# Performance work log

Measured on AMD Instinct MI355X. Metric: run time of the kernel, lower is better.

## Reference

```python
import jax, jax.numpy as jnp
import numpy as np

B, T1, S, M = 64, 129, 128, 32   # batch, time-major dim, seq_len, num_series
U = 256                           # SkipGRUUnits
SKIP = 4                          # skip
HW = 128                          # highway window (== S by shape constraints)


def _skip_lstm(x_seq, kernel, rkernel, kernel2, bias, bias2, s0, units, skip):
    """Run the bespoke skip-LSTM cell over time. x_seq: (B, T, D) -> (B, T, U)."""
    Bx = x_seq.shape[0]
    # precompute input projections for all timesteps: (B, T, 4U)
    xW = jnp.einsum('btd,du->btu', x_seq, kernel) + bias
    # recurrent kernel viewed per-gate: Rk[:, g, :] == rkernel[:, g*U:(g+1)*U]
    Rk = rkernel.reshape(units, 4, units)

    def step(carry, x_t):
        h_tm1, c_tm1, prev_h = carry            # (B,4U), (B,U), (B,U*skip)
        x_i, x_f, x_c, x_o = jnp.split(x_t, 4, axis=1)
        hg = h_tm1.reshape(Bx, 4, units)        # gate-specific previous state
        r = jnp.einsum('bgu,ugv->bgv', hg, Rk)  # (B,4,U)
        i = jax.nn.sigmoid(x_i + r[:, 0])
        f = jax.nn.sigmoid(x_f + r[:, 1])
        c = f * c_tm1 + i * jnp.tanh(x_c + r[:, 2])
        o = jax.nn.sigmoid(x_o + r[:, 3])
        h = o * jnp.tanh(c)
        h_skip = jax.nn.sigmoid(prev_h[:, :units] @ kernel2 + bias2)
        h = s0 * h + (1.0 - s0) * h_skip
        new_h_tm1 = jnp.concatenate([i, f, c, o], axis=1)
        new_prev = jnp.concatenate([prev_h[:, units:], h], axis=1)
        return (new_h_tm1, c, new_prev), h

    init = (jnp.zeros((Bx, 4 * units), x_seq.dtype),
            jnp.zeros((Bx, units), x_seq.dtype),
            jnp.zeros((Bx, units * skip), x_seq.dtype))
    _, hs = jax.lax.scan(step, init, jnp.swapaxes(xW, 0, 1))  # (T,B,U)
    return jnp.swapaxes(hs, 0, 1)


def setup_inputs() -> dict:
    key = jax.random.key(0)
    ks = jax.random.split(key, 10)
    g = lambda k, shape, s=0.05: (jax.random.normal(k, shape, jnp.float32) * s)
    return {
        'X': jax.random.normal(ks[0], (B, T1, S, M), jnp.float32),
        'enc_kernel': g(ks[1], (M, 4 * U)),
        'enc_rkernel': g(ks[2], (U, 4 * U)),
        'enc_kernel2': g(ks[3], (U, U)),
        'enc_bias': jnp.zeros((4 * U,), jnp.float32),
        'enc_bias2': jnp.zeros((U,), jnp.float32),
        'enc_s0': jnp.float32(0.5),
        'dec_kernel': g(ks[4], (U, 4 * U)),
        'dec_rkernel': g(ks[5], (U, 4 * U)),
        'dec_kernel2': g(ks[6], (U, U)),
        'dec_bias': jnp.zeros((4 * U,), jnp.float32),
        'dec_bias2': jnp.zeros((U,), jnp.float32),
        'dec_s0': jnp.float32(0.5),
        'dense_w': g(ks[7], (S * U, S * M), 0.01),
        'dense_b': jnp.zeros((S * M,), jnp.float32),
        'final_w': g(ks[8], (HW,), 0.05),
        'final_b': jnp.zeros((), jnp.float32),
    }


def reference(X, enc_kernel, enc_rkernel, enc_kernel2, enc_bias, enc_bias2, enc_s0,
              dec_kernel, dec_rkernel, dec_kernel2, dec_bias, dec_bias2, dec_s0,
              dense_w, dense_b, final_w, final_b):
    X1 = X[:, 0]        # (B, S, M) encoder input
    X2 = X[:, 1:]       # (B, T1-1, S, M) highway inputs
    SE = _skip_lstm(X1, enc_kernel, enc_rkernel, enc_kernel2, enc_bias, enc_bias2, enc_s0, U, SKIP)
    SD = _skip_lstm(SE, dec_kernel, dec_rkernel, dec_kernel2, dec_bias, dec_bias2, dec_s0, U, SKIP)
    RD = SD.reshape(X.shape[0], S * U)
    Y = (RD @ dense_w + dense_b).reshape(-1, S, M)  # (B, S, M)
    # highway: PreARTrans takes last HW steps, shared final Linear(S->1) over time axis
    Z2 = jnp.einsum('bism,s->bim', X2[:, :, -HW:, :], final_w) + final_b  # (B, T1-1, M)
    return Y + Z2
```

## Files before the change

### kernel.cpp

```cpp
#include <hip/hip_runtime.h>
#include <hip/hip_fp16.h>


__device__ __forceinline__ float sigmoidf_(float x) {
    return 1.0f / (1.0f + __expf(-x));
}
__device__ __forceinline__ float tanhf_(float x) {
    float xc = fminf(fmaxf(x, -15.f), 15.f);
    float e = __expf(2.f * xc);
    return (e - 1.f) / (e + 1.f);
}
__device__ __forceinline__ unsigned pkh(float lo, float hi) {
    __half2 h = __halves2half2(__float2half(lo), __float2half(hi));
    return *reinterpret_cast<unsigned*>(&h);
}
__device__ __forceinline__ float2 uph(unsigned u) {
    __half2 h = *reinterpret_cast<__half2*>(&u);
    return __half22float2(h);
}

__global__ __launch_bounds__(256) void packall(
    const float* __restrict__ e_rk, const float* __restrict__ d_rk,
    const float* __restrict__ d_k,  const float* __restrict__ e_k,
    const float* __restrict__ e_k2, const float* __restrict__ d_k2,
    float4* __restrict__ rk4e, float4* __restrict__ rk4d,
    float4* __restrict__ dk4,  float4* __restrict__ ek4,
    unsigned* __restrict__ kh2e, unsigned* __restrict__ kh2d,
    unsigned* __restrict__ flags)
{
    const int bx = blockIdx.x, v = threadIdx.x;
    if (bx < 800) {
        const float* src; float4* dst; int row;
        if (bx < 256)      { src = e_rk; dst = rk4e; row = bx; }
        else if (bx < 512) { src = d_rk; dst = rk4d; row = bx - 256; }
        else if (bx < 768) { src = d_k;  dst = dk4;  row = bx - 512; }
        else               { src = e_k;  dst = ek4;  row = bx - 768; }
        const float* s = src + (size_t)row * 1024;
        dst[row * 256 + v] = make_float4(s[v], s[256 + v], s[512 + v], s[768 + v]);
    } else if (bx < 928) {
        const int u2 = bx - 800;
        kh2e[u2 * 256 + v] = pkh(e_k2[(2 * u2) * 256 + v], e_k2[(2 * u2 + 1) * 256 + v]);
        kh2d[u2 * 256 + v] = pkh(d_k2[(2 * u2) * 256 + v], d_k2[(2 * u2 + 1) * 256 + v]);
    } else {
        flags[v] = 0u;
    }
}

__global__ __launch_bounds__(256) void xw_gemm_enc(
    const float*  __restrict__ X,
    const float4* __restrict__ ek4,
    const float*  __restrict__ bias,
    float4* __restrict__ xWp)
{
    const int v = threadIdx.x;
    const int r0 = blockIdx.x * 16;
    __shared__ float se[16][32];

    #pragma unroll
    for (int p = 0; p < 2; ++p) {
        int idx = p * 256 + v;
        int rr = idx >> 5, d = idx & 31;
        int R = r0 + rr, b = R >> 7, t = R & 127;
        se[rr][d] = X[((size_t)b * 129 * 128 + t) * 32 + d];
    }
    __syncthreads();

    float4 bv = make_float4(bias[v], bias[256 + v], bias[512 + v], bias[768 + v]);
    float4 acc[16];
    #pragma unroll
    for (int rr = 0; rr < 16; ++rr) acc[rr] = bv;

    #pragma unroll
    for (int u = 0; u < 32; ++u) {
        float4 w = ek4[u * 256 + v];
        #pragma unroll
        for (int rr = 0; rr < 16; ++rr) {
            float s = se[rr][u];
            acc[rr].x += s * w.x; acc[rr].y += s * w.y;
            acc[rr].z += s * w.z; acc[rr].w += s * w.w;
        }
    }
    #pragma unroll
    for (int rr = 0; rr < 16; ++rr)
        xWp[(size_t)(r0 + rr) * 256 + v] = acc[rr];
}

__global__ __launch_bounds__(512) void xw_gemm_dec(
    const float*  __restrict__ SE,
    const float4* __restrict__ dk4,
    const float*  __restrict__ bias,
    float4* __restrict__ xWp)
{
    const int tid = threadIdx.x;
    const int v = tid & 255;
    const int hh = tid >> 8;
    const int rbase = blockIdx.x * 32;
    __shared__ float se[32][256];

    for (int i = tid; i < 8192; i += 512) {
        int rr = i >> 8, c = i & 255;
        se[rr][c] = SE[(size_t)(rbase + rr) * 256 + c];
    }
    __syncthreads();

    float4 bv = make_float4(bias[v], bias[256 + v], bias[512 + v], bias[768 + v]);
    float4 acc[16];
    #pragma unroll
    for (int rr = 0; rr < 16; ++rr) acc[rr] = bv;

    #pragma unroll 8
    for (int u = 0; u < 256; ++u) {
        float4 w = dk4[u * 256 + v];
        #pragma unroll
        for (int rr = 0; rr < 16; ++rr) {
            float s = se[hh * 16 + rr][u];
            acc[rr].x += s * w.x; acc[rr].y += s * w.y;
            acc[rr].z += s * w.z; acc[rr].w += s * w.w;
        }
    }
    #pragma unroll
    for (int rr = 0; rr < 16; ++rr)
        xWp[(size_t)(rbase + hh * 16 + rr) * 256 + v] = acc[rr];
}

__global__ __launch_bounds__(1024, 4) void rec9(
    const float4*   __restrict__ xW,
    const float4*   __restrict__ rk4,
    const unsigned* __restrict__ kh2,
    const float*    __restrict__ bias2,
    const float*    __restrict__ s0p,
    float* __restrict__ out,
    float* __restrict__ EX,
    unsigned* __restrict__ flags,
    unsigned fbase)
{
    const int b     = blockIdx.x & 63;
    const int slice = blockIdx.x >> 6;
    const int voff  = slice * 64;
    const int tid   = threadIdx.x;
    const int us    = tid >> 6;
    const int vl    = tid & 63;
    const int v     = voff + vl;

    __shared__ float4 wres[128][64];
    __shared__ float4 pA[16][64];
    __shared__ float  pS[16][64];
    __shared__ float4 h4[256];
    __shared__ float  pq[4][256];

    for (int i = tid; i < 8192; i += 1024) {
        int r = i >> 6, vv = i & 63;
        int cc = r >> 3, j = r & 7;
        wres[r][vv] = rk4[(cc * 16 + j) * 256 + voff + vv];
    }
    float4 wreg[8];
    unsigned kreg[8];
    {
        const float4*   wp = rk4 + (us * 16 + 8) * 256 + v;
        const unsigned* kp = kh2 + (us * 8) * 256 + v;
        #pragma unroll
        for (int j = 0; j < 8; ++j) wreg[j] = wp[j * 256];
        #pragma unroll
        for (int j = 0; j < 8; ++j) kreg[j] = kp[j * 256];
    }
    if (tid < 256) {
        h4[tid] = make_float4(0.f, 0.f, 0.f, 0.f);
        pq[0][tid] = 0.f; pq[1][tid] = 0.f; pq[2][tid] = 0.f; pq[3][tid] = 0.f;
    }
    float cst = 0.f;
    const float s0 = s0p[0];
    const float b2 = bias2[voff + vl];
    unsigned* mflag = flags + b * 4 + slice;
    __syncthreads();

    for (int t = 0; t < 128; ++t) {
        float4 xa = make_float4(0.f, 0.f, 0.f, 0.f);
        if (tid < 64) xa = xW[((size_t)b * 128 + t) * 256 + voff + tid];
        if (t > 0 && tid < 3) {
            int ps = tid + (tid >= slice ? 1 : 0);
            const unsigned* pf = flags + b * 4 + ps;
            while (__hip_atomic_load(pf, __ATOMIC_RELAXED, __HIP_MEMORY_SCOPE_AGENT) < fbase + (unsigned)t)
                __builtin_amdgcn_s_sleep(2);
        }
        __syncthreads();
        if (t > 0) {
            const int sp = (t + 1) & 1;
            if (tid < 480) {
                int pi = tid / 160;
                int j  = tid - pi * 160;
                int ps = pi + (pi >= slice ? 1 : 0);
                const unsigned long long* src = (const unsigned long long*)
                    (EX + (((size_t)sp * 64 + b) * 4 + ps) * 320);
                unsigned long long d = __hip_atomic_load(src + j, __ATOMIC_RELAXED, __HIP_MEMORY_SCOPE_AGENT);
                if (j < 128) {
                    reinterpret_cast<unsigned long long*>(&h4[ps * 64])[j] = d;
                } else {
                    int k = j - 128;
                    union { unsigned long long u; float f[2]; } cv; cv.u = d;
                    pq[(t + 3) & 3][ps * 64 + 2 * k]     = cv.f[0];
                    pq[(t + 3) & 3][ps * 64 + 2 * k + 1] = cv.f[1];
                }
            }
        }
        __syncthreads();

        float ai = 0.f, af = 0.f, acg = 0.f, ao = 0.f, as = 0.f;
        const int slot = t & 3;
        #pragma unroll
        for (int j = 0; j < 8; ++j) {
            float4 w = wres[us * 8 + j][vl];
            float4 g = h4[us * 16 + j];
            ai += g.x * w.x; af += g.y * w.y; acg += g.z * w.z; ao += g.w * w.w;
        }
        #pragma unroll
        for (int j = 0; j < 8; ++j) {
            float4 w = wreg[j];
            float4 g = h4[us * 16 + 8 + j];
            ai += g.x * w.x; af += g.y * w.y; acg += g.z * w.z; ao += g.w * w.w;
        }
        #pragma unroll
        for (int j = 0; j < 8; ++j) {
            float2 kk = uph(kreg[j]);
            as += pq[slot][us * 16 + 2 * j] * kk.x + pq[slot][us * 16 + 2 * j + 1] * kk.y;
        }
        pA[us][vl] = make_float4(ai, af, acg, ao);
        pS[us][vl] = as;
        __syncthreads();

        if (tid < 64) {
            float4 A = pA[0][vl];
            float  S = pS[0][vl];
            #pragma unroll
            for (int cc = 1; cc < 16; ++cc) {
                float4 q = pA[cc][vl];
                A.x += q.x; A.y += q.y; A.z += q.z; A.w += q.w;
                S += pS[cc][vl];
            }
            float gi = sigmoidf_(xa.x + A.x);
            float gf = sigmoidf_(xa.y + A.y);
            float cb = tanhf_(xa.z + A.z);
            cst = gf * cst + gi * cb;
            float go = sigmoidf_(xa.w + A.w);
            float hh = go * tanhf_(cst);
            float hs = sigmoidf_(S + b2);
            float hf = s0 * hh + (1.f - s0) * hs;
            h4[voff + vl] = make_float4(gi, gf, cst, go);
            pq[slot][voff + vl] = hf;
            out[((size_t)b * 128 + t) * 256 + voff + vl] = hf;
            float* dst = EX + (((size_t)(t & 1) * 64 + b) * 4 + slice) * 320;
            union { float4 f4; unsigned long long u[2]; } gv;
            gv.f4 = make_float4(gi, gf, cst, go);
            __hip_atomic_store((unsigned long long*)dst + 2 * vl,     gv.u[0], __ATOMIC_RELAXED, __HIP_MEMORY_SCOPE_AGENT);
            __hip_atomic_store((unsigned long long*)dst + 2 * vl + 1, gv.u[1], __ATOMIC_RELAXED, __HIP_MEMORY_SCOPE_AGENT);
            __hip_atomic_store(dst + 256 + vl, hf, __ATOMIC_RELAXED, __HIP_MEMORY_SCOPE_AGENT);
        }
        __syncthreads();
        if (tid == 0)
            __hip_atomic_store(mflag, fbase + (unsigned)(t + 1), __ATOMIC_RELAXED, __HIP_MEMORY_SCOPE_AGENT);
    }
}

__global__ __launch_bounds__(512, 4) void dense3(
    const float* __restrict__ SD,
    const float* __restrict__ dw,
    float* __restrict__ P)
{
    const int bid = blockIdx.x;
    const int kc = bid >> 5;
    const int bb = (bid >> 3) & 3;
    const int ct = bid & 7;
    const int tid = threadIdx.x;
    const int wv  = tid >> 6;
    const int wvj = wv & 1;
    const int wv2 = wv >> 1;
    const int lane = tid & 63;
    const int j0 = ct * 512 + wvj * 256 + lane * 4;
    const int kbase = kc * 2048;

    __shared__ float sst[16][68];
    __shared__ float red[4][4][520];

    float4 acc[16];
    #pragma unroll
    for (int b = 0; b < 16; ++b) acc[b] = make_float4(0.f, 0.f, 0.f, 0.f);

    for (int k0 = 0; k0 < 2048; k0 += 64) {
        if (tid < 256) {
            int r = tid >> 4, c4 = (tid & 15) * 4;
            float4 s4 = *reinterpret_cast<const float4*>(
                SD + (size_t)(bb * 16 + r) * 32768 + kbase + k0 + c4);
            sst[r][c4] = s4.x; sst[r][c4 + 1] = s4.y; sst[r][c4 + 2] = s4.z; sst[r][c4 + 3] = s4.w;
        }
        __syncthreads();
        #pragma unroll 2
        for (int kk = 0; kk < 16; ++kk) {
            const int krel = kk * 4 + wv2;
            float4 w4 = *reinterpret_cast<const float4*>(
                dw + (size_t)(kbase + k0 + krel) * 4096 + j0);
            #pragma unroll
            for (int b = 0; b < 16; ++b) {
                float s = sst[b][krel];
                acc[b].x += s * w4.x; acc[b].y += s * w4.y;
                acc[b].z += s * w4.z; acc[b].w += s * w4.w;
            }
        }
        __syncthreads();
    }

    for (int bg = 0; bg < 4; ++bg) {
        __syncthreads();
        #pragma unroll
        for (int i = 0; i < 4; ++i) {
            float4 a = acc[bg * 4 + i];
            float* d = &red[wv2][i][wvj * 256 + lane * 4];
            d[0] = a.x; d[1] = a.y; d[2] = a.z; d[3] = a.w;
        }
        __syncthreads();
        {
            int bi = tid >> 7;
            int jj = (tid & 127) * 4;
            float4 s;
            s.x = red[0][bi][jj]     + red[1][bi][jj]     + red[2][bi][jj]     + red[3][bi][jj];
            s.y = red[0][bi][jj + 1] + red[1][bi][jj + 1] + red[2][bi][jj + 1] + red[3][bi][jj + 1];
            s.z = red[0][bi][jj + 2] + red[1][bi][jj + 2] + red[2][bi][jj + 2] + red[3][bi][jj + 2];
            s.w = red[0][bi][jj + 3] + red[1][bi][jj + 3] + red[2][bi][jj + 3] + red[3][bi][jj + 3];
            *reinterpret_cast<float4*>(
                P + ((size_t)(kc * 64 + bb * 16 + bg * 4 + bi) * 4096) + ct * 512 + jj) = s;
        }
    }
}

__global__ __launch_bounds__(256) void reduce_z2(
    const float* __restrict__ P,
    const float* __restrict__ db,
    const float* __restrict__ X,
    const float* __restrict__ fw,
    const float* __restrict__ fbp,
    float* __restrict__ out)
{
    const int o4 = blockIdx.x * 256 + threadIdx.x;
    const int b  = o4 >> 10;
    const int j4 = o4 & 1023;
    const int j0 = j4 * 4;
    const int i  = j0 >> 5;
    const int m  = j0 & 31;

    float4 acc = *reinterpret_cast<const float4*>(db + j0);
    #pragma unroll
    for (int kc = 0; kc < 16; ++kc) {
        float4 p = *reinterpret_cast<const float4*>(P + (size_t)(kc * 64 + b) * 4096 + j0);
        acc.x += p.x; acc.y += p.y; acc.z += p.z; acc.w += p.w;
    }

    const float* xp = X + ((size_t)(b * 129 + 1 + i) * 128) * 32 + m;
    #pragma unroll 8
    for (int s = 0; s < 128; ++s) {
        float4 xv = *reinterpret_cast<const float4*>(xp + (size_t)s * 32);
        float w = fw[s];
        acc.x += w * xv.x; acc.y += w * xv.y; acc.z += w * xv.z; acc.w += w * xv.w;
    }
    const float fb = fbp[0];
    acc.x += fb; acc.y += fb; acc.z += fb; acc.w += fb;
    *reinterpret_cast<float4*>(out + (size_t)o4 * 4) = acc;
}

extern "C" void kernel_launch(void* const* d_in, const int* in_sizes, int n_in,
                              void* d_out, int out_size, void* d_ws, size_t ws_size,
                              hipStream_t stream) {
    const float* X    = (const float*)d_in[0];
    const float* e_k  = (const float*)d_in[1];
    const float* e_rk = (const float*)d_in[2];
    const float* e_k2 = (const float*)d_in[3];
    const float* e_b  = (const float*)d_in[4];
    const float* e_b2 = (const float*)d_in[5];
    const float* e_s0 = (const float*)d_in[6];
    const float* d_k  = (const float*)d_in[7];
    const float* d_rk = (const float*)d_in[8];
    const float* d_k2 = (const float*)d_in[9];
    const float* d_b  = (const float*)d_in[10];
    const float* d_b2 = (const float*)d_in[11];
    const float* d_s0 = (const float*)d_in[12];
    const float* dw   = (const float*)d_in[13];
    const float* db   = (const float*)d_in[14];
    const float* fw   = (const float*)d_in[15];
    const float* fb   = (const float*)d_in[16];

    float* ws = (float*)d_ws;
    float4*   rk4e  = (float4*)(ws);
    float4*   rk4d  = (float4*)(ws + 262144);
    float4*   dk4   = (float4*)(ws + 524288);
    float4*   ek4   = (float4*)(ws + 786432);
    unsigned* kh2e  = (unsigned*)(ws + 819200);
    unsigned* kh2d  = (unsigned*)(ws + 851968);
    float*    EX    = ws + 884736;
    unsigned* flags = (unsigned*)(ws + 1212416);
    float*    xW    = ws + 1310720;
    float*    SE    = ws + 9699328;
    float*    SD    = ws + 11796480;

    float* P = xW;

    hipLaunchKernelGGL(packall, dim3(929), dim3(256), 0, stream,
                       e_rk, d_rk, d_k, e_k, e_k2, d_k2,
                       rk4e, rk4d, dk4, ek4, kh2e, kh2d, flags);
    hipLaunchKernelGGL(xw_gemm_enc, dim3(512), dim3(256), 0, stream,
                       X, ek4, e_b, (float4*)xW);
    hipLaunchKernelGGL(rec9, dim3(256), dim3(1024), 0, stream,
                       (const float4*)xW, rk4e, kh2e, e_b2, e_s0, SE, EX, flags, 0u);
    hipLaunchKernelGGL(xw_gemm_dec, dim3(256), dim3(512), 0, stream,
                       SE, dk4, d_b, (float4*)xW);
    hipLaunchKernelGGL(rec9, dim3(256), dim3(1024), 0, stream,
                       (const float4*)xW, rk4d, kh2d, d_b2, d_s0, SD, EX, flags, 128u);
    hipLaunchKernelGGL(dense3, dim3(512), dim3(512), 0, stream, SD, dw, P);
    hipLaunchKernelGGL(reduce_z2, dim3(256), dim3(256), 0, stream,
                       P, db, X, fw, fb, (float*)d_out);
}
```

Before: 1.191 ms.

## Split recurrence across 8 blocks per batch pair and interleave two batches

The recurrent kernel now gives each block two batch elements and a 32-column slice, so each batch is spread over 8 blocks instead of 4. Work for the two batches is software-pipelined: while one batch's gate update and state exchange are in flight, the other batch's matvec runs. The aim is to hide cross-block flag waits and global exchange latency behind compute. It also moves most recurrent weights and the packed skip kernel into shared memory and replaces the block-wide wait with per-producer readiness flags in shared memory. The cost is more producers per batch to synchronise with and more complex spin-wait logic.

```diff
diff --git a/kernel.cpp b/kernel.cpp
--- a/kernel.cpp
+++ b/kernel.cpp
@@ -42,7 +42,7 @@
         kh2e[u2 * 256 + v] = pkh(e_k2[(2 * u2) * 256 + v], e_k2[(2 * u2 + 1) * 256 + v]);
         kh2d[u2 * 256 + v] = pkh(d_k2[(2 * u2) * 256 + v], d_k2[(2 * u2 + 1) * 256 + v]);
     } else {
-        flags[v] = 0u;
+        flags[(bx - 928) * 256 + v] = 0u;
     }
 }
 
@@ -123,7 +123,7 @@
         xWp[(size_t)(rbase + hh * 16 + rr) * 256 + v] = acc[rr];
 }
 
-__global__ __launch_bounds__(1024, 4) void rec9(
+__global__ __launch_bounds__(1024, 4) void rec10(
     const float4*   __restrict__ xW,
     const float4*   __restrict__ rk4,
     const unsigned* __restrict__ kh2,
@@ -134,129 +134,167 @@
     unsigned* __restrict__ flags,
     unsigned fbase)
 {
-    const int b     = blockIdx.x & 63;
-    const int slice = blockIdx.x >> 6;
-    const int voff  = slice * 64;
+    const int p     = blockIdx.x & 31;
+    const int slice = blockIdx.x >> 5;
+    const int voff  = slice * 32;
     const int tid   = threadIdx.x;
-    const int us    = tid >> 6;
-    const int vl    = tid & 63;
+    const int uc    = tid >> 5;
+    const int vl    = tid & 31;
     const int v     = voff + vl;
-
-    __shared__ float4 wres[128][64];
-    __shared__ float4 pA[16][64];
-    __shared__ float  pS[16][64];
-    __shared__ float4 h4[256];
-    __shared__ float  pq[4][256];
-
-    for (int i = tid; i < 8192; i += 1024) {
-        int r = i >> 6, vv = i & 63;
-        int cc = r >> 3, j = r & 7;
-        wres[r][vv] = rk4[(cc * 16 + j) * 256 + voff + vv];
-    }
+    const int b0    = 2 * p, b1 = 2 * p + 1;
+
+    __shared__ float4   wres[192][32];
+    __shared__ unsigned kh2l[128][32];
+    __shared__ float4   h4[2][256];
+    __shared__ float    pq[2][4][256];
+    __shared__ float4   pA[32][33];
+    __shared__ float    pS[32][33];
+    __shared__ unsigned sready[2][8];
+
+    for (int i = tid; i < 6144; i += 1024) {
+        int r = i >> 5, vv = i & 31;
+        wres[r][vv] = rk4[r * 256 + voff + vv];
+    }
+    for (int i = tid; i < 4096; i += 1024) {
+        int r = i >> 5, vv = i & 31;
+        kh2l[r][vv] = kh2[r * 256 + voff + vv];
+    }
+    if (tid < 512) {
+        int c = tid >> 8, u = tid & 255;
+        h4[c][u] = make_float4(0.f, 0.f, 0.f, 0.f);
+        pq[c][0][u] = 0.f; pq[c][1][u] = 0.f; pq[c][2][u] = 0.f; pq[c][3][u] = 0.f;
+    }
+    if (tid < 16) sready[tid >> 3][tid & 7] = 0u;
+
     float4 wreg[8];
-    unsigned kreg[8];
-    {
-        const float4*   wp = rk4 + (us * 16 + 8) * 256 + v;
-        const unsigned* kp = kh2 + (us * 8) * 256 + v;
-        #pragma unroll
-        for (int j = 0; j < 8; ++j) wreg[j] = wp[j * 256];
-        #pragma unroll
-        for (int j = 0; j < 8; ++j) kreg[j] = kp[j * 256];
-    }
-    if (tid < 256) {
-        h4[tid] = make_float4(0.f, 0.f, 0.f, 0.f);
-        pq[0][tid] = 0.f; pq[1][tid] = 0.f; pq[2][tid] = 0.f; pq[3][tid] = 0.f;
-    }
-    float cst = 0.f;
+    if (uc >= 24) {
+        #pragma unroll
+        for (int j = 0; j < 8; ++j)
+            wreg[j] = rk4[(uc * 8 + j) * 256 + v];
+    }
+    float cst0 = 0.f, cst1 = 0.f;
+    float4 xa0 = make_float4(0.f,0.f,0.f,0.f), xa1 = xa0;
     const float s0 = s0p[0];
-    const float b2 = bias2[voff + vl];
-    unsigned* mflag = flags + b * 4 + slice;
+    const float b2 = bias2[v];
     __syncthreads();
 
     for (int t = 0; t < 128; ++t) {
-        float4 xa = make_float4(0.f, 0.f, 0.f, 0.f);
-        if (tid < 64) xa = xW[((size_t)b * 128 + t) * 256 + voff + tid];
-        if (t > 0 && tid < 3) {
-            int ps = tid + (tid >= slice ? 1 : 0);
-            const unsigned* pf = flags + b * 4 + ps;
-            while (__hip_atomic_load(pf, __ATOMIC_RELAXED, __HIP_MEMORY_SCOPE_AGENT) < fbase + (unsigned)t)
-                __builtin_amdgcn_s_sleep(2);
-        }
-        __syncthreads();
-        if (t > 0) {
-            const int sp = (t + 1) & 1;
-            if (tid < 480) {
-                int pi = tid / 160;
-                int j  = tid - pi * 160;
-                int ps = pi + (pi >= slice ? 1 : 0);
-                const unsigned long long* src = (const unsigned long long*)
-                    (EX + (((size_t)sp * 64 + b) * 4 + ps) * 320);
-                unsigned long long d = __hip_atomic_load(src + j, __ATOMIC_RELAXED, __HIP_MEMORY_SCOPE_AGENT);
-                if (j < 128) {
-                    reinterpret_cast<unsigned long long*>(&h4[ps * 64])[j] = d;
-                } else {
-                    int k = j - 128;
-                    union { unsigned long long u; float f[2]; } cv; cv.u = d;
-                    pq[(t + 3) & 3][ps * 64 + 2 * k]     = cv.f[0];
-                    pq[(t + 3) & 3][ps * 64 + 2 * k + 1] = cv.f[1];
+        #pragma unroll
+        for (int c = 0; c < 2; ++c) {
+            const int bc = 2 * p + c;
+            const int bo = 2 * p + (c ^ 1);
+            if (tid < 32) {
+                const int tf = t - (c == 0 ? 1 : 0);
+                if (tf >= 0) {
+                    float4 A = pA[0][tid]; float S = pS[0][tid];
+                    #pragma unroll
+                    for (int cc = 1; cc < 32; ++cc) {
+                        float4 q = pA[cc][tid];
+                        A.x += q.x; A.y += q.y; A.z += q.z; A.w += q.w;
+                        S += pS[cc][tid];
+                    }
+                    float4 xa = (c == 0) ? xa1 : xa0;
+                    float gi = sigmoidf_(xa.x + A.x);
+                    float gf = sigmoidf_(xa.y + A.y);
+                    float cb = tanhf_(xa.z + A.z);
+                    float cstn = gf * ((c == 0) ? cst1 : cst0) + gi * cb;
+                    if (c == 0) cst1 = cstn; else cst0 = cstn;
+                    float go = sigmoidf_(xa.w + A.w);
+                    float hh = go * tanhf_(cstn);
+                    float hs = sigmoidf_(S + b2);
+                    float hf = s0 * hh + (1.f - s0) * hs;
+                    h4[c ^ 1][voff + tid] = make_float4(gi, gf, cstn, go);
+                    pq[c ^ 1][tf & 3][voff + tid] = hf;
+                    out[((size_t)bo * 128 + tf) * 256 + voff + tid] = hf;
+                    float* dst = EX + (((size_t)(tf & 1) * 64 + bo) * 8 + slice) * 160;
+                    union { float4 f4; unsigned long long u[2]; } gv;
+                    gv.f4 = make_float4(gi, gf, cstn, go);
+                    __hip_atomic_store((unsigned long long*)dst + 2 * tid,     gv.u[0], __ATOMIC_RELAXED, __HIP_MEMORY_SCOPE_AGENT);
+                    __hip_atomic_store((unsigned long long*)dst + 2 * tid + 1, gv.u[1], __ATOMIC_RELAXED, __HIP_MEMORY_SCOPE_AGENT);
+                    __hip_atomic_store((unsigned*)(dst + 128) + tid, __float_as_uint(hf), __ATOMIC_RELAXED, __HIP_MEMORY_SCOPE_AGENT);
+                    asm volatile("s_waitcnt vmcnt(0)" ::: "memory");
+                    if (tid == 0)
+                        __hip_atomic_store(flags + bo * 8 + slice, fbase + (unsigned)(tf + 1),
+                                           __ATOMIC_RELAXED, __HIP_MEMORY_SCOPE_AGENT);
+                }
+                float4 x = xW[((size_t)bc * 128 + t) * 256 + voff + tid];
+                if (c == 0) xa0 = x; else xa1 = x;
+            } else if (t > 0) {
+                const int st = tid - 64;
+                const unsigned T = fbase + (unsigned)t;
+                if (tid >= 64 && st < 7) {
+                    int ps = st + (st >= slice ? 1 : 0);
+                    const unsigned* pf = flags + bc * 8 + ps;
+                    while (__hip_atomic_load(pf, __ATOMIC_RELAXED, __HIP_MEMORY_SCOPE_AGENT) < T)
+                        __builtin_amdgcn_s_sleep(1);
+                    __hip_atomic_store(&sready[c][ps], T, __ATOMIC_RELAXED, __HIP_MEMORY_SCOPE_WORKGROUP);
+                }
+                if (tid >= 64 && st < 560) {
+                    int pi = st / 80, j = st - pi * 80;
+                    int ps = pi + (pi >= slice ? 1 : 0);
+                    while (__hip_atomic_load(&sready[c][ps], __ATOMIC_RELAXED, __HIP_MEMORY_SCOPE_WORKGROUP) < T)
+                        __builtin_amdgcn_s_sleep(1);
+                    const unsigned long long* src = (const unsigned long long*)
+                        (EX + (((size_t)((t + 1) & 1) * 64 + bc) * 8 + ps) * 160);
+                    unsigned long long d = __hip_atomic_load(src + j, __ATOMIC_RELAXED, __HIP_MEMORY_SCOPE_AGENT);
+                    if (j < 64) {
+                        ((unsigned long long*)&h4[c][0])[ps * 64 + j] = d;
+                    } else {
+                        int k = j - 64;
+                        union { unsigned long long u; float f[2]; } cv; cv.u = d;
+                        pq[c][(t + 3) & 3][ps * 32 + 2 * k]     = cv.f[0];
+                        pq[c][(t + 3) & 3][ps * 32 + 2 * k + 1] = cv.f[1];
+                    }
                 }
             }
-        }
-        __syncthreads();
-
-        float ai = 0.f, af = 0.f, acg = 0.f, ao = 0.f, as = 0.f;
-        const int slot = t & 3;
-        #pragma unroll
-        for (int j = 0; j < 8; ++j) {
-            float4 w = wres[us * 8 + j][vl];
-            float4 g = h4[us * 16 + j];
-            ai += g.x * w.x; af += g.y * w.y; acg += g.z * w.z; ao += g.w * w.w;
-        }
-        #pragma unroll
-        for (int j = 0; j < 8; ++j) {
-            float4 w = wreg[j];
-            float4 g = h4[us * 16 + 8 + j];
-            ai += g.x * w.x; af += g.y * w.y; acg += g.z * w.z; ao += g.w * w.w;
-        }
-        #pragma unroll
-        for (int j = 0; j < 8; ++j) {
-            float2 kk = uph(kreg[j]);
-            as += pq[slot][us * 16 + 2 * j] * kk.x + pq[slot][us * 16 + 2 * j + 1] * kk.y;
-        }
-        pA[us][vl] = make_float4(ai, af, acg, ao);
-        pS[us][vl] = as;
-        __syncthreads();
-
-        if (tid < 64) {
-            float4 A = pA[0][vl];
-            float  S = pS[0][vl];
-            #pragma unroll
-            for (int cc = 1; cc < 16; ++cc) {
-                float4 q = pA[cc][vl];
-                A.x += q.x; A.y += q.y; A.z += q.z; A.w += q.w;
-                S += pS[cc][vl];
+            __syncthreads();
+            {
+                const int slot = t & 3;
+                const int u0 = uc * 8;
+                float ai = 0.f, af = 0.f, ac = 0.f, ao = 0.f, as = 0.f;
+                if (uc < 24) {
+                    #pragma unroll
+                    for (int j = 0; j < 8; ++j) {
+                        float4 w = wres[u0 + j][vl];
+                        float4 g = h4[c][u0 + j];
+                        ai += g.x * w.x; af += g.y * w.y; ac += g.z * w.z; ao += g.w * w.w;
+                    }
+                } else {
+                    #pragma unroll
+                    for (int j = 0; j < 8; ++j) {
+                        float4 w = wreg[j];
+                        float4 g = h4[c][u0 + j];
+                        ai += g.x * w.x; af += g.y * w.y; ac += g.z * w.z; ao += g.w * w.w;
+                    }
+                }
+                #pragma unroll
+                for (int jp = 0; jp < 4; ++jp) {
+                    float2 kk = uph(kh2l[uc * 4 + jp][vl]);
+                    as += pq[c][slot][u0 + 2 * jp] * kk.x + pq[c][slot][u0 + 2 * jp + 1] * kk.y;
+                }
+                pA[uc][vl] = make_float4(ai, af, ac, ao);
+                pS[uc][vl] = as;
             }
-            float gi = sigmoidf_(xa.x + A.x);
-            float gf = sigmoidf_(xa.y + A.y);
-            float cb = tanhf_(xa.z + A.z);
-            cst = gf * cst + gi * cb;
-            float go = sigmoidf_(xa.w + A.w);
-            float hh = go * tanhf_(cst);
-            float hs = sigmoidf_(S + b2);
-            float hf = s0 * hh + (1.f - s0) * hs;
-            h4[voff + vl] = make_float4(gi, gf, cst, go);
-            pq[slot][voff + vl] = hf;
-            out[((size_t)b * 128 + t) * 256 + voff + vl] = hf;
-            float* dst = EX + (((size_t)(t & 1) * 64 + b) * 4 + slice) * 320;
-            union { float4 f4; unsigned long long u[2]; } gv;
-            gv.f4 = make_float4(gi, gf, cst, go);
-            __hip_atomic_store((unsigned long long*)dst + 2 * vl,     gv.u[0], __ATOMIC_RELAXED, __HIP_MEMORY_SCOPE_AGENT);
-            __hip_atomic_store((unsigned long long*)dst + 2 * vl + 1, gv.u[1], __ATOMIC_RELAXED, __HIP_MEMORY_SCOPE_AGENT);
-            __hip_atomic_store(dst + 256 + vl, hf, __ATOMIC_RELAXED, __HIP_MEMORY_SCOPE_AGENT);
-        }
-        __syncthreads();
-        if (tid == 0)
-            __hip_atomic_store(mflag, fbase + (unsigned)(t + 1), __ATOMIC_RELAXED, __HIP_MEMORY_SCOPE_AGENT);
+            __syncthreads();
+        }
+    }
+    if (tid < 32) {
+        float4 A = pA[0][tid]; float S = pS[0][tid];
+        #pragma unroll
+        for (int cc = 1; cc < 32; ++cc) {
+            float4 q = pA[cc][tid];
+            A.x += q.x; A.y += q.y; A.z += q.z; A.w += q.w;
+            S += pS[cc][tid];
+        }
+        float gi = sigmoidf_(xa1.x + A.x);
+        float gf = sigmoidf_(xa1.y + A.y);
+        float cb = tanhf_(xa1.z + A.z);
+        cst1 = gf * cst1 + gi * cb;
+        float go = sigmoidf_(xa1.w + A.w);
+        float hh = go * tanhf_(cst1);
+        float hs = sigmoidf_(S + b2);
+        float hf = s0 * hh + (1.f - s0) * hs;
+        out[((size_t)b1 * 128 + 127) * 256 + voff + tid] = hf;
     }
 }
 
@@ -393,24 +431,24 @@
     unsigned* kh2e  = (unsigned*)(ws + 819200);
     unsigned* kh2d  = (unsigned*)(ws + 851968);
     float*    EX    = ws + 884736;
-    unsigned* flags = (unsigned*)(ws + 1212416);
+    unsigned* flags = (unsigned*)(ws + 1048576);
     float*    xW    = ws + 1310720;
     float*    SE    = ws + 9699328;
     float*    SD    = ws + 11796480;
 
     float* P = xW;
 
-    hipLaunchKernelGGL(packall, dim3(929), dim3(256), 0, stream,
+    hipLaunchKernelGGL(packall, dim3(930), dim3(256), 0, stream,
                        e_rk, d_rk, d_k, e_k, e_k2, d_k2,
                        rk4e, rk4d, dk4, ek4, kh2e, kh2d, flags);
     hipLaunchKernelGGL(xw_gemm_enc, dim3(512), dim3(256), 0, stream,
                        X, ek4, e_b, (float4*)xW);
-    hipLaunchKernelGGL(rec9, dim3(256), dim3(1024), 0, stream,
+    hipLaunchKernelGGL(rec10, dim3(256), dim3(1024), 0, stream,
                        (const float4*)xW, rk4e, kh2e, e_b2, e_s0, SE, EX, flags, 0u);
     hipLaunchKernelGGL(xw_gemm_dec, dim3(256), dim3(512), 0, stream,
                        SE, dk4, d_b, (float4*)xW);
-    hipLaunchKernelGGL(rec9, dim3(256), dim3(1024), 0, stream,
-                       (const float4*)xW, rk4d, kh2d, d_b2, d_s0, SD, EX, flags, 128u);
+    hipLaunchKernelGGL(rec10, dim3(256), dim3(1024), 0, stream,
+                       (const float4*)xW, rk4d, kh2d, d_b2, d_s0, SD, EX, flags, 1000u);
     hipLaunchKernelGGL(dense3, dim3(512), dim3(512), 0, stream, SD, dw, P);
     hipLaunchKernelGGL(reduce_z2, dim3(256), dim3(256), 0, stream,
                        P, db, X, fw, fb, (float*)d_out);
```

New measurement: 1.605 ms. 1.35x slower.

## Double-buffer SD tile and prefetch dense weights in registers

Applied to the files above, without the earlier changes.

The dense GEMM kernel now double-buffers the SD activation tile in shared memory, so the next chunk loads while the current one is computed, removing one barrier per iteration. It also keeps 8 float4 weight rows in flight in registers and issues each load ahead of the FMAs that consume it, to hide global memory latency on the large weight stream. The cost is more shared memory and higher register pressure under launch_bounds(512,4), which could cause spills or lower occupancy.

```diff
diff --git a/kernel.cpp b/kernel.cpp
--- a/kernel.cpp
+++ b/kernel.cpp
@@ -260,7 +260,7 @@
     }
 }
 
-__global__ __launch_bounds__(512, 4) void dense3(
+__global__ __launch_bounds__(512, 4) void dense4(
     const float* __restrict__ SD,
     const float* __restrict__ dw,
     float* __restrict__ P)
@@ -277,31 +277,56 @@
     const int j0 = ct * 512 + wvj * 256 + lane * 4;
     const int kbase = kc * 2048;
 
-    __shared__ float sst[16][68];
+    __shared__ float sst[2][16][68];
     __shared__ float red[4][4][520];
 
     float4 acc[16];
     #pragma unroll
     for (int b = 0; b < 16; ++b) acc[b] = make_float4(0.f, 0.f, 0.f, 0.f);
 
-    for (int k0 = 0; k0 < 2048; k0 += 64) {
-        if (tid < 256) {
-            int r = tid >> 4, c4 = (tid & 15) * 4;
+    const int sr = tid >> 4, sc4 = (tid & 15) * 4;
+    if (tid < 256) {
+        float4 s4 = *reinterpret_cast<const float4*>(
+            SD + (size_t)(bb * 16 + sr) * 32768 + kbase + sc4);
+        float* d = &sst[0][sr][0];
+        d[sc4] = s4.x; d[sc4 + 1] = s4.y; d[sc4 + 2] = s4.z; d[sc4 + 3] = s4.w;
+    }
+    __syncthreads();
+
+    for (int it = 0; it < 32; ++it) {
+        const int buf = it & 1;
+        const int k0 = it * 64;
+        if (it < 31 && tid < 256) {
             float4 s4 = *reinterpret_cast<const float4*>(
-                SD + (size_t)(bb * 16 + r) * 32768 + kbase + k0 + c4);
-            sst[r][c4] = s4.x; sst[r][c4 + 1] = s4.y; sst[r][c4 + 2] = s4.z; sst[r][c4 + 3] = s4.w;
-        }
-        __syncthreads();
-        #pragma unroll 2
-        for (int kk = 0; kk < 16; ++kk) {
-            const int krel = kk * 4 + wv2;
-            float4 w4 = *reinterpret_cast<const float4*>(
-                dw + (size_t)(kbase + k0 + krel) * 4096 + j0);
+                SD + (size_t)(bb * 16 + sr) * 32768 + kbase + k0 + 64 + sc4);
+            float* d = &sst[buf ^ 1][sr][0];
+            d[sc4] = s4.x; d[sc4 + 1] = s4.y; d[sc4 + 2] = s4.z; d[sc4 + 3] = s4.w;
+        }
+        const float* wrow = dw + (size_t)(kbase + k0 + wv2) * 4096 + j0;
+        float4 wa[4], wb[4];
+        #pragma unroll
+        for (int q = 0; q < 4; ++q)
+            wa[q] = *reinterpret_cast<const float4*>(wrow + (size_t)(q * 4) * 4096);
+        #pragma unroll
+        for (int q = 0; q < 4; ++q)
+            wb[q] = *reinterpret_cast<const float4*>(wrow + (size_t)(16 + q * 4) * 4096);
+        #pragma unroll
+        for (int g = 0; g < 4; ++g) {
             #pragma unroll
-            for (int b = 0; b < 16; ++b) {
-                float s = sst[b][krel];
-                acc[b].x += s * w4.x; acc[b].y += s * w4.y;
-                acc[b].z += s * w4.z; acc[b].w += s * w4.w;
+            for (int q = 0; q < 4; ++q) {
+                const int krel = (g * 4 + q) * 4 + wv2;
+                float4 w4 = (g & 1) ? wb[q] : wa[q];
+                #pragma unroll
+                for (int b = 0; b < 16; ++b) {
+                    float s = sst[buf][b][krel];
+                    acc[b].x += s * w4.x; acc[b].y += s * w4.y;
+                    acc[b].z += s * w4.z; acc[b].w += s * w4.w;
+                }
+                if (g < 2) {
+                    float4 nw = *reinterpret_cast<const float4*>(
+                        wrow + (size_t)((g + 2) * 16 + q * 4) * 4096);
+                    if (g & 1) wb[q] = nw; else wa[q] = nw;
+                }
             }
         }
         __syncthreads();
@@ -411,7 +436,7 @@
                        SE, dk4, d_b, (float4*)xW);
     hipLaunchKernelGGL(rec9, dim3(256), dim3(1024), 0, stream,
                        (const float4*)xW, rk4d, kh2d, d_b2, d_s0, SD, EX, flags, 128u);
-    hipLaunchKernelGGL(dense3, dim3(512), dim3(512), 0, stream, SD, dw, P);
+    hipLaunchKernelGGL(dense4, dim3(512), dim3(512), 0, stream, SD, dw, P);
     hipLaunchKernelGGL(reduce_z2, dim3(256), dim3(256), 0, stream,
                        P, db, X, fw, fb, (float*)d_out);
 }
```

Result: no change. 1.207 ms (+1.3%).

## Replace block-wide barriers with per-slice LDS ready flags in recurrent kernel

Applied to the files above, without the earlier changes.

The recurrent kernel stops using two __syncthreads per step around the cross-block exchange. One polling wave spins on the peer flags and publishes a per-peer ready value in shared memory. Each group of four waves that consumes a given peer's slice waits only on that peer's flag, loads the data, and then starts its partial dot products. The producer wave now publishes its own flag right after a vmcnt wait, which drops one more barrier. The aim is to cut per-step barrier latency on this serial 128-step chain, at the cost of busy-wait spinning and reliance on LDS memory-ordering subtleties.

```diff
diff --git a/kernel.cpp b/kernel.cpp
--- a/kernel.cpp
+++ b/kernel.cpp
@@ -123,7 +123,7 @@
         xWp[(size_t)(rbase + hh * 16 + rr) * 256 + v] = acc[rr];
 }
 
-__global__ __launch_bounds__(1024, 4) void rec9(
+__global__ __launch_bounds__(1024, 4) void rec11(
     const float4*   __restrict__ xW,
     const float4*   __restrict__ rk4,
     const unsigned* __restrict__ kh2,
@@ -141,12 +141,16 @@
     const int us    = tid >> 6;
     const int vl    = tid & 63;
     const int v     = voff + vl;
+    const int reg   = us >> 2;
+    const bool own  = (reg == slice);
+    const int lane  = vl;
 
     __shared__ float4 wres[128][64];
     __shared__ float4 pA[16][64];
     __shared__ float  pS[16][64];
     __shared__ float4 h4[256];
     __shared__ float  pq[4][256];
+    __shared__ unsigned sready[4];
 
     for (int i = tid; i < 8192; i += 1024) {
         int r = i >> 6, vv = i & 63;
@@ -167,64 +171,70 @@
         h4[tid] = make_float4(0.f, 0.f, 0.f, 0.f);
         pq[0][tid] = 0.f; pq[1][tid] = 0.f; pq[2][tid] = 0.f; pq[3][tid] = 0.f;
     }
+    if (tid < 4) sready[tid] = fbase;
     float cst = 0.f;
     const float s0 = s0p[0];
     const float b2 = bias2[voff + vl];
     unsigned* mflag = flags + b * 4 + slice;
+    const bool pollwave = (us == slice * 4 + 1);
     __syncthreads();
 
     for (int t = 0; t < 128; ++t) {
+        const unsigned T = fbase + (unsigned)t;
         float4 xa = make_float4(0.f, 0.f, 0.f, 0.f);
         if (tid < 64) xa = xW[((size_t)b * 128 + t) * 256 + voff + tid];
-        if (t > 0 && tid < 3) {
-            int ps = tid + (tid >= slice ? 1 : 0);
-            const unsigned* pf = flags + b * 4 + ps;
-            while (__hip_atomic_load(pf, __ATOMIC_RELAXED, __HIP_MEMORY_SCOPE_AGENT) < fbase + (unsigned)t)
-                __builtin_amdgcn_s_sleep(2);
-        }
-        __syncthreads();
+
         if (t > 0) {
-            const int sp = (t + 1) & 1;
-            if (tid < 480) {
-                int pi = tid / 160;
-                int j  = tid - pi * 160;
-                int ps = pi + (pi >= slice ? 1 : 0);
-                const unsigned long long* src = (const unsigned long long*)
-                    (EX + (((size_t)sp * 64 + b) * 4 + ps) * 320);
-                unsigned long long d = __hip_atomic_load(src + j, __ATOMIC_RELAXED, __HIP_MEMORY_SCOPE_AGENT);
-                if (j < 128) {
-                    reinterpret_cast<unsigned long long*>(&h4[ps * 64])[j] = d;
-                } else {
-                    int k = j - 128;
-                    union { unsigned long long u; float f[2]; } cv; cv.u = d;
-                    pq[(t + 3) & 3][ps * 64 + 2 * k]     = cv.f[0];
-                    pq[(t + 3) & 3][ps * 64 + 2 * k + 1] = cv.f[1];
+            if (pollwave && lane < 3) {
+                int ps = lane + (lane >= slice ? 1 : 0);
+                const unsigned* pf = flags + b * 4 + ps;
+                while (__hip_atomic_load(pf, __ATOMIC_RELAXED, __HIP_MEMORY_SCOPE_AGENT) < T) { }
+                __hip_atomic_store(&sready[ps], T, __ATOMIC_RELAXED, __HIP_MEMORY_SCOPE_WORKGROUP);
+            }
+            if (!own) {
+                while (__hip_atomic_load(&sready[reg], __ATOMIC_RELAXED, __HIP_MEMORY_SCOPE_WORKGROUP) < T)
+                    __builtin_amdgcn_s_sleep(1);
+                const int sp = (t + 1) & 1;
+                const float* srcf = EX + (((size_t)sp * 64 + b) * 4 + reg) * 320;
+                if (lane < 32) {
+                    const unsigned long long* src = (const unsigned long long*)srcf;
+                    int jj = (us & 3) * 32 + lane;
+                    unsigned long long d = __hip_atomic_load(src + jj, __ATOMIC_RELAXED, __HIP_MEMORY_SCOPE_AGENT);
+                    reinterpret_cast<unsigned long long*>(&h4[reg * 64])[(us & 3) * 32 + lane] = d;
+                } else if (lane < 48) {
+                    int k = lane - 32;
+                    int uu = (us & 3) * 16 + k;
+                    unsigned hv = __hip_atomic_load((const unsigned*)(srcf + 256) + uu,
+                                                    __ATOMIC_RELAXED, __HIP_MEMORY_SCOPE_AGENT);
+                    pq[(t + 3) & 3][reg * 64 + uu] = __uint_as_float(hv);
                 }
-            }
-        }
-        __syncthreads();
-
-        float ai = 0.f, af = 0.f, acg = 0.f, ao = 0.f, as = 0.f;
-        const int slot = t & 3;
-        #pragma unroll
-        for (int j = 0; j < 8; ++j) {
-            float4 w = wres[us * 8 + j][vl];
-            float4 g = h4[us * 16 + j];
-            ai += g.x * w.x; af += g.y * w.y; acg += g.z * w.z; ao += g.w * w.w;
-        }
-        #pragma unroll
-        for (int j = 0; j < 8; ++j) {
-            float4 w = wreg[j];
-            float4 g = h4[us * 16 + 8 + j];
-            ai += g.x * w.x; af += g.y * w.y; acg += g.z * w.z; ao += g.w * w.w;
-        }
-        #pragma unroll
-        for (int j = 0; j < 8; ++j) {
-            float2 kk = uph(kreg[j]);
-            as += pq[slot][us * 16 + 2 * j] * kk.x + pq[slot][us * 16 + 2 * j + 1] * kk.y;
-        }
-        pA[us][vl] = make_float4(ai, af, acg, ao);
-        pS[us][vl] = as;
+                asm volatile("s_waitcnt vmcnt(0) lgkmcnt(0)" ::: "memory");
+            }
+        }
+
+        {
+            float ai = 0.f, af = 0.f, acg = 0.f, ao = 0.f, as = 0.f;
+            const int slot = t & 3;
+            #pragma unroll
+            for (int j = 0; j < 8; ++j) {
+                float4 w = wres[us * 8 + j][vl];
+                float4 g = h4[us * 16 + j];
+                ai += g.x * w.x; af += g.y * w.y; acg += g.z * w.z; ao += g.w * w.w;
+            }
+            #pragma unroll
+            for (int j = 0; j < 8; ++j) {
+                float4 w = wreg[j];
+                float4 g = h4[us * 16 + 8 + j];
+                ai += g.x * w.x; af += g.y * w.y; acg += g.z * w.z; ao += g.w * w.w;
+            }
+            #pragma unroll
+            for (int j = 0; j < 8; ++j) {
+                float2 kk = uph(kreg[j]);
+                as += pq[slot][us * 16 + 2 * j] * kk.x + pq[slot][us * 16 + 2 * j + 1] * kk.y;
+            }
+            pA[us][vl] = make_float4(ai, af, acg, ao);
+            pS[us][vl] = as;
+        }
         __syncthreads();
 
         if (tid < 64) {
@@ -245,18 +255,19 @@
             float hs = sigmoidf_(S + b2);
             float hf = s0 * hh + (1.f - s0) * hs;
             h4[voff + vl] = make_float4(gi, gf, cst, go);
-            pq[slot][voff + vl] = hf;
+            pq[t & 3][voff + vl] = hf;
             out[((size_t)b * 128 + t) * 256 + voff + vl] = hf;
             float* dst = EX + (((size_t)(t & 1) * 64 + b) * 4 + slice) * 320;
             union { float4 f4; unsigned long long u[2]; } gv;
             gv.f4 = make_float4(gi, gf, cst, go);
             __hip_atomic_store((unsigned long long*)dst + 2 * vl,     gv.u[0], __ATOMIC_RELAXED, __HIP_MEMORY_SCOPE_AGENT);
             __hip_atomic_store((unsigned long long*)dst + 2 * vl + 1, gv.u[1], __ATOMIC_RELAXED, __HIP_MEMORY_SCOPE_AGENT);
-            __hip_atomic_store(dst + 256 + vl, hf, __ATOMIC_RELAXED, __HIP_MEMORY_SCOPE_AGENT);
-        }
-        __syncthreads();
-        if (tid == 0)
-            __hip_atomic_store(mflag, fbase + (unsigned)(t + 1), __ATOMIC_RELAXED, __HIP_MEMORY_SCOPE_AGENT);
+            __hip_atomic_store((unsigned*)(dst + 256) + vl, __float_as_uint(hf), __ATOMIC_RELAXED, __HIP_MEMORY_SCOPE_AGENT);
+            asm volatile("s_waitcnt vmcnt(0)" ::: "memory");
+            if (tid == 0)
+                __hip_atomic_store(mflag, T + 1u, __ATOMIC_RELAXED, __HIP_MEMORY_SCOPE_AGENT);
+        }
+        __syncthreads();
     }
 }
 
@@ -405,11 +416,11 @@
                        rk4e, rk4d, dk4, ek4, kh2e, kh2d, flags);
     hipLaunchKernelGGL(xw_gemm_enc, dim3(512), dim3(256), 0, stream,
                        X, ek4, e_b, (float4*)xW);
-    hipLaunchKernelGGL(rec9, dim3(256), dim3(1024), 0, stream,
+    hipLaunchKernelGGL(rec11, dim3(256), dim3(1024), 0, stream,
                        (const float4*)xW, rk4e, kh2e, e_b2, e_s0, SE, EX, flags, 0u);
     hipLaunchKernelGGL(xw_gemm_dec, dim3(256), dim3(512), 0, stream,
                        SE, dk4, d_b, (float4*)xW);
-    hipLaunchKernelGGL(rec9, dim3(256), dim3(1024), 0, stream,
+    hipLaunchKernelGGL(rec11, dim3(256), dim3(1024), 0, stream,
                        (const float4*)xW, rk4d, kh2d, d_b2, d_s0, SD, EX, flags, 128u);
     hipLaunchKernelGGL(dense3, dim3(512), dim3(512), 0, stream, SD, dw, P);
     hipLaunchKernelGGL(reduce_z2, dim3(256), dim3(256), 0, stream,
```

After: 1.463 ms. 22.9% more time.
